# Kernel tuning notes

Measured on AMD Instinct MI355X. Metric: run time of the kernel, lower is better.

Reference implementation:

```python
import jax, jax.numpy as jnp
import numpy as np

MODES = 16
WIDTH = 64
SCHMIDT = 8
N_LAYERS = 4


def _spectral_conv(x, wr, wi, modes):
    """Quantum spectral conv: truncated 2D FFT -> complex Schmidt-rank einsum -> inverse FFT.
    x: (B,H,W,C) real. wr, wi: (modes,modes,C,C,S)."""
    b, H, W, C = x.shape
    S = wr.shape[-1]
    # quantum_fourier_modes: keep low (modes x modes) Fourier modes
    x_ft = jnp.fft.fftn(x, axes=(1, 2))[:, :modes, :modes, :]          # (B,m,n,C) complex
    w = wr + 1j * wi                                                     # (m,n,C,C,S)
    # tensor_product_einsum('b...nc,mncos->b...mos')
    out_ft = jnp.einsum('bxnc,mncos->bxmos', x_ft, w)                   # (B,m,m,C,S)
    # recombine Schmidt components (normalized sum over rank)
    out_ft = out_ft.sum(axis=-1) * (1.0 / float(np.sqrt(S)))            # (B,m,m,C)
    full = jnp.zeros((b, H, W, C), dtype=x_ft.dtype).at[:, :modes, :modes, :].set(out_ft)
    # inverse quantum_fourier_modes + .real
    return jnp.fft.ifftn(full, axes=(1, 2)).real


def setup_inputs() -> dict:
    key = jax.random.key(0)
    ks = jax.random.split(key, 12)
    B, H, W, Cin = 16, 128, 128, 3
    sc = 0.02
    inp = {
        'x': jax.random.normal(ks[0], (B, H, W, Cin), jnp.float32),
        'fc_in_w': jax.random.normal(ks[1], (Cin, WIDTH), jnp.float32) * sc,
        'fc_in_b': jnp.zeros((WIDTH,), jnp.float32),
        'wr': jax.random.normal(ks[2], (N_LAYERS, MODES, MODES, WIDTH, WIDTH, SCHMIDT), jnp.float32) * sc,
        'wi': jax.random.normal(ks[3], (N_LAYERS, MODES, MODES, WIDTH, WIDTH, SCHMIDT), jnp.float32) * sc,
        'ww': jax.random.normal(ks[4], (N_LAYERS, WIDTH, WIDTH), jnp.float32) * sc,
        'wb': jnp.zeros((N_LAYERS, WIDTH), jnp.float32),
        'fc1_w': jax.random.normal(ks[5], (WIDTH, 128), jnp.float32) * sc,
        'fc1_b': jnp.zeros((128,), jnp.float32),
        'fc2_w': jax.random.normal(ks[6], (128, 1), jnp.float32) * sc,
        'fc2_b': jnp.zeros((1,), jnp.float32),
    }
    return inp


def reference(x, fc_in_w, fc_in_b, wr, wi, ww, wb, fc1_w, fc1_b, fc2_w, fc2_b) -> jnp.ndarray:
    h = x @ fc_in_w + fc_in_b                                   # (B,H,W,width)
    for i in range(N_LAYERS):
        x1 = _spectral_conv(h, wr[i], wi[i], MODES)             # quantum spectral path
        x2 = h @ ww[i] + wb[i]                                  # pointwise Dense path
        h = jax.nn.gelu(x1 + x2)
    h = jax.nn.gelu(h @ fc1_w + fc1_b)
    return h @ fc2_w + fc2_b                                    # (B,H,W,1)
```

## Files before the change

### kernel.cpp

```cpp
#include <hip/hip_runtime.h>
#include <math.h>


#define TWO_PI_128 0.049087385212340517f
#define PI_4       0.78539816339744831f

__device__ __forceinline__ float gelu_f(float v) {
  float ex = 1.5957691216057308f * v * fmaf(0.044715f, v * v, 1.0f);
  float e = __expf(fminf(ex, 30.0f));
  float r = __builtin_amdgcn_rcpf(e + 1.0f);
  return fmaf(-v, r, v);
}

__global__ __launch_bounds__(256) void k_fc_in(const float* __restrict__ x,
    const float* __restrict__ w, const float* __restrict__ b,
    float* __restrict__ h) {
  int t = blockIdx.x * 256 + threadIdx.x;
  int pix = t >> 4, c4 = (t & 15) << 2;
  float x0 = x[pix * 3], x1 = x[pix * 3 + 1], x2 = x[pix * 3 + 2];
  float4 acc = *(const float4*)&b[c4];
  float4 w0 = *(const float4*)&w[c4];
  float4 w1 = *(const float4*)&w[64 + c4];
  float4 w2 = *(const float4*)&w[128 + c4];
  acc.x = fmaf(x2, w2.x, fmaf(x1, w1.x, fmaf(x0, w0.x, acc.x)));
  acc.y = fmaf(x2, w2.y, fmaf(x1, w1.y, fmaf(x0, w0.y, acc.y)));
  acc.z = fmaf(x2, w2.z, fmaf(x1, w1.z, fmaf(x0, w0.z, acc.z)));
  acc.w = fmaf(x2, w2.w, fmaf(x1, w1.w, fmaf(x0, w0.w, acc.w)));
  *(float4*)&h[(size_t)pix * 64 + c4] = acc;
}

__global__ __launch_bounds__(256) void k_prep(const float* __restrict__ wr,
    const float* __restrict__ wi, float* __restrict__ Br, float* __restrict__ Bi) {
  int t = blockIdx.x * 256 + threadIdx.x;
  int o = t & 63, c = (t >> 6) & 63, n = (t >> 12) & 15, m = t >> 16;
  const float4* pr = (const float4*)(wr) + (size_t)t * 2;
  float4 a = pr[0], d = pr[1];
  float sr = ((a.x + a.y) + (a.z + a.w)) + ((d.x + d.y) + (d.z + d.w));
  const float4* pi = (const float4*)(wi) + (size_t)t * 2;
  a = pi[0]; d = pi[1];
  float si = ((a.x + a.y) + (a.z + a.w)) + ((d.x + d.y) + (d.z + d.w));
  const float scale = 0.35355339059327373f / 16384.0f;
  int k = n * 64 + c, j = m * 64 + o;
  Br[k * 1024 + j] = sr * scale;
  Bi[k * 1024 + j] = si * scale;
}

__global__ __launch_bounds__(256) void k_dft_y(const float* __restrict__ h,
                                               float2* __restrict__ A1) {
  __shared__ float sh[128 * 64];
  int bx = blockIdx.x;
  const float* src = h + (size_t)bx * 8192;
  for (int i = threadIdx.x; i < 2048; i += 256)
    *(float4*)&sh[i * 4] = *(const float4*)&src[i * 4];
  __syncthreads();
  int c = threadIdx.x & 63, kg = threadIdx.x >> 6;
  float cs[4], sn[4], wr_[4], wi_[4], sr[4], si[4];
  #pragma unroll
  for (int q = 0; q < 4; ++q) {
    int ky = kg + 4 * q;
    __sincosf(-TWO_PI_128 * (float)ky, &sn[q], &cs[q]);
    wr_[q] = 1.f; wi_[q] = 0.f; sr[q] = 0.f; si[q] = 0.f;
  }
  for (int y = 0; y < 128; ++y) {
    float hv = sh[y * 64 + c];
    #pragma unroll
    for (int q = 0; q < 4; ++q) {
      sr[q] = fmaf(hv, wr_[q], sr[q]);
      si[q] = fmaf(hv, wi_[q], si[q]);
      float nw = wr_[q] * cs[q] - wi_[q] * sn[q];
      wi_[q] = fmaf(wi_[q], cs[q], wr_[q] * sn[q]);
      wr_[q] = nw;
    }
  }
  #pragma unroll
  for (int q = 0; q < 4; ++q) {
    int ky = kg + 4 * q;
    A1[((size_t)bx * 16 + ky) * 64 + c] = make_float2(sr[q], si[q]);
  }
}

__global__ __launch_bounds__(256) void k_dft_x(const float2* __restrict__ A1,
    float* __restrict__ Ar, float* __restrict__ Ai) {
  __shared__ float2 sh[128 * 32];
  int b = blockIdx.x, ky = blockIdx.y, ch = blockIdx.z;
  int c0 = ch * 32;
  for (int i = threadIdx.x; i < 2048; i += 256) {
    int xx = i >> 4, u = (i & 15) * 2;
    *(float4*)&sh[xx * 32 + u] =
        *(const float4*)&A1[(((size_t)b * 128 + xx) * 16 + ky) * 64 + c0 + u];
  }
  __syncthreads();
  int cl = threadIdx.x & 31, kxg = threadIdx.x >> 5;
  float cs[2], sn[2], wr_[2], wi_[2], sr[2], si[2];
  #pragma unroll
  for (int q = 0; q < 2; ++q) {
    int kx = kxg + 8 * q;
    __sincosf(-TWO_PI_128 * (float)kx, &sn[q], &cs[q]);
    wr_[q] = 1.f; wi_[q] = 0.f; sr[q] = 0.f; si[q] = 0.f;
  }
  for (int xx = 0; xx < 128; ++xx) {
    float2 v = sh[xx * 32 + cl];
    #pragma unroll
    for (int q = 0; q < 2; ++q) {
      sr[q] = fmaf(v.x, wr_[q], sr[q]); sr[q] = fmaf(-v.y, wi_[q], sr[q]);
      si[q] = fmaf(v.x, wi_[q], si[q]); si[q] = fmaf(v.y, wr_[q], si[q]);
      float nw = wr_[q] * cs[q] - wi_[q] * sn[q];
      wi_[q] = fmaf(wi_[q], cs[q], wr_[q] * sn[q]);
      wr_[q] = nw;
    }
  }
  #pragma unroll
  for (int q = 0; q < 2; ++q) {
    int kx = kxg + 8 * q;
    int row = b * 16 + kx, col = ky * 64 + c0 + cl;
    Ar[row * 1024 + col] = sr[q];
    Ai[row * 1024 + col] = si[q];
  }
}

__global__ __launch_bounds__(256) void k_gemm(const float* __restrict__ Ar,
    const float* __restrict__ Ai, const float* __restrict__ Br,
    const float* __restrict__ Bi, float2* __restrict__ Cp) {
  __shared__ float2 As[32][34];
  __shared__ float2 Bs[32][34];
  int tx = threadIdx.x & 15, ty = threadIdx.x >> 4;
  int row0 = blockIdx.y * 32, col0 = blockIdx.x * 32, kbase = blockIdx.z * 512;
  float cr00 = 0, cr01 = 0, cr10 = 0, cr11 = 0;
  float ci00 = 0, ci01 = 0, ci10 = 0, ci11 = 0;
  for (int kt = 0; kt < 512; kt += 32) {
    int k0 = kbase + kt;
    {
      int r = threadIdx.x >> 3, k4 = (threadIdx.x & 7) << 2;
      int gi = (row0 + r) * 1024 + k0 + k4;
      float4 ar = *(const float4*)&Ar[gi];
      float4 ai = *(const float4*)&Ai[gi];
      *(float4*)&As[r][k4]     = make_float4(ar.x, ai.x, ar.y, ai.y);
      *(float4*)&As[r][k4 + 2] = make_float4(ar.z, ai.z, ar.w, ai.w);
    }
    {
      int kk = threadIdx.x >> 3, j4 = (threadIdx.x & 7) << 2;
      int gi = (k0 + kk) * 1024 + col0 + j4;
      float4 br = *(const float4*)&Br[gi];
      float4 bi = *(const float4*)&Bi[gi];
      *(float4*)&Bs[kk][j4]     = make_float4(br.x, bi.x, br.y, bi.y);
      *(float4*)&Bs[kk][j4 + 2] = make_float4(br.z, bi.z, br.w, bi.w);
    }
    __syncthreads();
    #pragma unroll 8
    for (int kk = 0; kk < 32; ++kk) {
      float2 a0 = As[ty * 2][kk], a1 = As[ty * 2 + 1][kk];
      float2 b0 = Bs[kk][tx * 2], b1 = Bs[kk][tx * 2 + 1];
      cr00 = fmaf(a0.x, b0.x, cr00); cr00 = fmaf(-a0.y, b0.y, cr00);
      ci00 = fmaf(a0.x, b0.y, ci00); ci00 = fmaf(a0.y, b0.x, ci00);
      cr01 = fmaf(a0.x, b1.x, cr01); cr01 = fmaf(-a0.y, b1.y, cr01);
      ci01 = fmaf(a0.x, b1.y, ci01); ci01 = fmaf(a0.y, b1.x, ci01);
      cr10 = fmaf(a1.x, b0.x, cr10); cr10 = fmaf(-a1.y, b0.y, cr10);
      ci10 = fmaf(a1.x, b0.y, ci10); ci10 = fmaf(a1.y, b0.x, ci10);
      cr11 = fmaf(a1.x, b1.x, cr11); cr11 = fmaf(-a1.y, b1.y, cr11);
      ci11 = fmaf(a1.x, b1.y, ci11); ci11 = fmaf(a1.y, b1.x, ci11);
    }
    __syncthreads();
  }
  int r = row0 + ty * 2, jj = col0 + tx * 2;
  size_t base = ((size_t)blockIdx.z * 256 + r) * 1024 + jj;
  Cp[base]        = make_float2(cr00, ci00);
  Cp[base + 1]    = make_float2(cr01, ci01);
  Cp[base + 1024] = make_float2(cr10, ci10);
  Cp[base + 1025] = make_float2(cr11, ci11);
}

__global__ __launch_bounds__(256) void k_ifft_y(const float2* __restrict__ Cp,
                                                float2* __restrict__ T) {
  __shared__ float2 Cl[1024];
  int b = blockIdx.x >> 4, kx = blockIdx.x & 15;
  int row = b * 16 + kx;
  for (int i = threadIdx.x; i < 512; i += 256) {
    float4 u = *(const float4*)&Cp[(size_t)row * 1024 + i * 2];
    float4 v = *(const float4*)&Cp[(size_t)(256 + row) * 1024 + i * 2];
    *(float4*)&Cl[i * 2] = make_float4(u.x + v.x, u.y + v.y, u.z + v.z, u.w + v.w);
  }
  __syncthreads();
  int c = threadIdx.x & 63, yg = threadIdx.x >> 6;
  for (int y = yg; y < 128; y += 4) {
    float snv, csv;
    __sincosf(TWO_PI_128 * (float)y, &snv, &csv);
    float wr_ = 1.f, wi_ = 0.f, sr = 0.f, si = 0.f;
    #pragma unroll
    for (int ky = 0; ky < 16; ++ky) {
      float2 v = Cl[ky * 64 + c];
      sr = fmaf(v.x, wr_, sr); sr = fmaf(-v.y, wi_, sr);
      si = fmaf(v.x, wi_, si); si = fmaf(v.y, wr_, si);
      float nw = wr_ * csv - wi_ * snv;
      wi_ = fmaf(wi_, csv, wr_ * snv);
      wr_ = nw;
    }
    T[(((size_t)b * 128 + y) * 16 + kx) * 64 + c] = make_float2(sr, si);
  }
}

__global__ __launch_bounds__(256, 4) void k_layer_out(const float* hin,
    const float2* __restrict__ T, const float* __restrict__ ww,
    const float* __restrict__ wb, float* hout) {
  __shared__ alignas(16) float wwT[64 * 68];
  int b = blockIdx.x >> 7, y = blockIdx.x & 127;
  for (int i = threadIdx.x; i < 1024; i += 256) {
    int k = i >> 4, c4 = (i & 15) << 2;
    float4 v = *(const float4*)&ww[k * 64 + c4];
    wwT[(c4 + 0) * 68 + k] = v.x;
    wwT[(c4 + 1) * 68 + k] = v.y;
    wwT[(c4 + 2) * 68 + k] = v.z;
    wwT[(c4 + 3) * 68 + k] = v.w;
  }
  const float2* Tp = T + ((size_t)b * 128 + y) * 1024;
  __syncthreads();
  int ct = threadIdx.x & 15, xg = threadIdx.x >> 4;
  float acc[8][4];
  #pragma unroll
  for (int cc = 0; cc < 4; ++cc) {
    float bv = wb[ct + 16 * cc];
    #pragma unroll
    for (int j = 0; j < 8; ++j) acc[j][cc] = bv;
  }
  for (int kx = 0; kx < 16; ++kx) {
    float tr[4], ti[4];
    #pragma unroll
    for (int cc = 0; cc < 4; ++cc) {
      float2 v = Tp[kx * 64 + ct + 16 * cc];
      tr[cc] = v.x; ti[cc] = v.y;
    }
    float s0v, c0v, sst, cst;
    __sincosf(TWO_PI_128 * (float)(kx * xg), &s0v, &c0v);
    __sincosf(PI_4 * (float)kx, &sst, &cst);
    float wr_ = c0v, wi_ = s0v;
    #pragma unroll
    for (int j = 0; j < 8; ++j) {
      #pragma unroll
      for (int cc = 0; cc < 4; ++cc) {
        acc[j][cc] = fmaf(tr[cc], wr_, acc[j][cc]);
        acc[j][cc] = fmaf(-ti[cc], wi_, acc[j][cc]);
      }
      float nw = wr_ * cst - wi_ * sst;
      wi_ = fmaf(wi_, cst, wr_ * sst);
      wr_ = nw;
    }
  }
  const float* hrow = hin + (((size_t)b * 128 + xg) * 128 + y) * 64;
  #pragma unroll 1
  for (int kq = 0; kq < 64; kq += 4) {
    float4 wv[4];
    #pragma unroll
    for (int cc = 0; cc < 4; ++cc)
      wv[cc] = *(const float4*)&wwT[(ct + 16 * cc) * 68 + kq];
    #pragma unroll
    for (int j = 0; j < 8; ++j) {
      float4 hv = *(const float4*)&hrow[(size_t)j * 131072 + kq];
      #pragma unroll
      for (int cc = 0; cc < 4; ++cc) {
        acc[j][cc] = fmaf(hv.x, wv[cc].x, acc[j][cc]);
        acc[j][cc] = fmaf(hv.y, wv[cc].y, acc[j][cc]);
        acc[j][cc] = fmaf(hv.z, wv[cc].z, acc[j][cc]);
        acc[j][cc] = fmaf(hv.w, wv[cc].w, acc[j][cc]);
      }
    }
  }
  __syncthreads();
  #pragma unroll
  for (int j = 0; j < 8; ++j) {
    int xx = xg + 16 * j;
    size_t base = (((size_t)b * 128 + xx) * 128 + y) * 64 + ct;
    #pragma unroll
    for (int cc = 0; cc < 4; ++cc)
      hout[base + 16 * cc] = gelu_f(acc[j][cc]);
  }
}

__global__ __launch_bounds__(256, 3) void k_final(const float* __restrict__ h,
    const float* __restrict__ w1, const float* __restrict__ b1,
    const float* __restrict__ w2, const float* __restrict__ b2,
    float* __restrict__ out) {
  __shared__ alignas(16) float w1T[128 * 68];
  __shared__ float b1s[128];
  __shared__ float w2s[128];
  for (int i = threadIdx.x; i < 2048; i += 256) {
    int k = i >> 5, j4 = (i & 31) << 2;
    float4 v = *(const float4*)&w1[k * 128 + j4];
    w1T[(j4 + 0) * 68 + k] = v.x;
    w1T[(j4 + 1) * 68 + k] = v.y;
    w1T[(j4 + 2) * 68 + k] = v.z;
    w1T[(j4 + 3) * 68 + k] = v.w;
  }
  if (threadIdx.x < 128) {
    b1s[threadIdx.x] = b1[threadIdx.x];
    w2s[threadIdx.x] = w2[threadIdx.x];
  }
  __syncthreads();
  int jt = threadIdx.x & 15, rg = threadIdx.x >> 4;
  int r0 = blockIdx.x * 128;
  const float* hb = h + (size_t)(r0 + rg) * 64;
  float acc[8][8];
  #pragma unroll
  for (int cc = 0; cc < 8; ++cc) {
    float bv = b1s[jt + 16 * cc];
    #pragma unroll
    for (int ii = 0; ii < 8; ++ii) acc[ii][cc] = bv;
  }
  float4 hv[8], hn[8];
  #pragma unroll
  for (int ii = 0; ii < 8; ++ii) hv[ii] = *(const float4*)&hb[ii * 1024];

  auto fmab = [&](const float4* H, int kq) {
    #pragma unroll
    for (int cc = 0; cc < 8; ++cc) {
      float4 wv = *(const float4*)&w1T[(jt + 16 * cc) * 68 + kq];
      #pragma unroll
      for (int ii = 0; ii < 8; ++ii) {
        acc[ii][cc] = fmaf(H[ii].x, wv.x, acc[ii][cc]);
        acc[ii][cc] = fmaf(H[ii].y, wv.y, acc[ii][cc]);
        acc[ii][cc] = fmaf(H[ii].z, wv.z, acc[ii][cc]);
        acc[ii][cc] = fmaf(H[ii].w, wv.w, acc[ii][cc]);
      }
    }
  };
  #pragma unroll 1
  for (int kq = 0; kq < 64; kq += 8) {
    #pragma unroll
    for (int ii = 0; ii < 8; ++ii)
      hn[ii] = *(const float4*)&hb[ii * 1024 + kq + 4];
    fmab(hv, kq);
    #pragma unroll
    for (int ii = 0; ii < 8; ++ii)
      hv[ii] = *(const float4*)&hb[ii * 1024 + kq + 8];
    fmab(hn, kq + 4);
  }
  float b2v = b2[0];
  #pragma unroll
  for (int ii = 0; ii < 8; ++ii) {
    float part = 0.f;
    #pragma unroll
    for (int cc = 0; cc < 8; ++cc)
      part = fmaf(gelu_f(acc[ii][cc]), w2s[jt + 16 * cc], part);
    part += __shfl_xor(part, 1, 64);
    part += __shfl_xor(part, 2, 64);
    part += __shfl_xor(part, 4, 64);
    part += __shfl_xor(part, 8, 64);
    if (jt == 0) out[r0 + rg + 16 * ii] = part + b2v;
  }
}

extern "C" void kernel_launch(void* const* d_in, const int* in_sizes, int n_in,
                              void* d_out, int out_size, void* d_ws, size_t ws_size,
                              hipStream_t stream) {
  (void)in_sizes; (void)n_in; (void)out_size; (void)ws_size;
  const float* x      = (const float*)d_in[0];
  const float* fcin_w = (const float*)d_in[1];
  const float* fcin_b = (const float*)d_in[2];
  const float* wr     = (const float*)d_in[3];
  const float* wi     = (const float*)d_in[4];
  const float* ww     = (const float*)d_in[5];
  const float* wb     = (const float*)d_in[6];
  const float* fc1_w  = (const float*)d_in[7];
  const float* fc1_b  = (const float*)d_in[8];
  const float* fc2_w  = (const float*)d_in[9];
  const float* fc2_b  = (const float*)d_in[10];
  float* out = (float*)d_out;

  float*  hA = (float*)d_ws;
  float2* A1 = (float2*)(hA + 16777216);
  float*  Ar = (float*)(A1 + 2097152);
  float*  Ai = Ar + 262144;
  float*  Br = Ai + 262144;
  float*  Bi = Br + 1048576;
  float2* Cp = (float2*)(Bi + 1048576);

  k_fc_in<<<16384, 256, 0, stream>>>(x, fcin_w, fcin_b, hA);
  for (int l = 0; l < 4; ++l) {
    k_prep<<<4096, 256, 0, stream>>>(wr + (size_t)l * 8388608,
                                     wi + (size_t)l * 8388608, Br, Bi);
    k_dft_y<<<2048, 256, 0, stream>>>(hA, A1);
    k_dft_x<<<dim3(16, 16, 2), 256, 0, stream>>>(A1, Ar, Ai);
    k_gemm<<<dim3(32, 8, 2), 256, 0, stream>>>(Ar, Ai, Br, Bi, Cp);
    k_ifft_y<<<256, 256, 0, stream>>>(Cp, A1);
    k_layer_out<<<2048, 256, 0, stream>>>(hA, A1, ww + (size_t)l * 4096,
                                          wb + (size_t)l * 64, hA);
  }
  k_final<<<2048, 256, 0, stream>>>(hA, fc1_w, fc1_b, fc2_w, fc2_b, out);
}
```

Before: 1.115 ms.

## Radix-4 split y-DFT, double-buffer complex GEMM tiles, stage h in LDS for final MLP

The y-direction DFT kernel now splits the 128-point sum into four interleaved 32-point partial sums that share one twiddle recurrence, then combines them with a small radix-4 twiddle step. This cuts the per-sample twiddle rotation work by about four times at the cost of more live registers. The complex GEMM gains a double-buffered LDS tile with register prefetch of the next K slice, so global loads overlap the FMA loop. The final MLP kernel stages its 128-row h tile into padded LDS with coalesced loads instead of strided per-thread register prefetch, and drops the occupancy hint from its launch bounds.

```diff
diff --git a/kernel.cpp b/kernel.cpp
--- a/kernel.cpp
+++ b/kernel.cpp
@@ -54,28 +54,48 @@
     *(float4*)&sh[i * 4] = *(const float4*)&src[i * 4];
   __syncthreads();
   int c = threadIdx.x & 63, kg = threadIdx.x >> 6;
-  float cs[4], sn[4], wr_[4], wi_[4], sr[4], si[4];
+  float s4r[4][4], s4i[4][4];
+  float w4r[4], w4i[4], c4t[4], s4t[4];
   #pragma unroll
   for (int q = 0; q < 4; ++q) {
     int ky = kg + 4 * q;
-    __sincosf(-TWO_PI_128 * (float)ky, &sn[q], &cs[q]);
-    wr_[q] = 1.f; wi_[q] = 0.f; sr[q] = 0.f; si[q] = 0.f;
-  }
-  for (int y = 0; y < 128; ++y) {
-    float hv = sh[y * 64 + c];
+    __sincosf(-TWO_PI_128 * 4.0f * (float)ky, &s4t[q], &c4t[q]);
+    w4r[q] = 1.f; w4i[q] = 0.f;
+    #pragma unroll
+    for (int p = 0; p < 4; ++p) { s4r[q][p] = 0.f; s4i[q][p] = 0.f; }
+  }
+  for (int m = 0; m < 32; ++m) {
+    float hv[4];
+    #pragma unroll
+    for (int p = 0; p < 4; ++p) hv[p] = sh[(4 * m + p) * 64 + c];
     #pragma unroll
     for (int q = 0; q < 4; ++q) {
-      sr[q] = fmaf(hv, wr_[q], sr[q]);
-      si[q] = fmaf(hv, wi_[q], si[q]);
-      float nw = wr_[q] * cs[q] - wi_[q] * sn[q];
-      wi_[q] = fmaf(wi_[q], cs[q], wr_[q] * sn[q]);
-      wr_[q] = nw;
+      #pragma unroll
+      for (int p = 0; p < 4; ++p) {
+        s4r[q][p] = fmaf(hv[p], w4r[q], s4r[q][p]);
+        s4i[q][p] = fmaf(hv[p], w4i[q], s4i[q][p]);
+      }
+      float nw = w4r[q] * c4t[q] - w4i[q] * s4t[q];
+      w4i[q] = fmaf(w4i[q], c4t[q], w4r[q] * s4t[q]);
+      w4r[q] = nw;
     }
   }
   #pragma unroll
   for (int q = 0; q < 4; ++q) {
     int ky = kg + 4 * q;
-    A1[((size_t)bx * 16 + ky) * 64 + c] = make_float2(sr[q], si[q]);
+    float s1, c1;
+    __sincosf(-TWO_PI_128 * (float)ky, &s1, &c1);
+    float sr = s4r[q][0], si = s4i[q][0];
+    float wr_ = c1, wi_ = s1;
+    #pragma unroll
+    for (int p = 1; p < 4; ++p) {
+      sr = fmaf(s4r[q][p], wr_, sr); sr = fmaf(-s4i[q][p], wi_, sr);
+      si = fmaf(s4r[q][p], wi_, si); si = fmaf(s4i[q][p], wr_, si);
+      float nw = wr_ * c1 - wi_ * s1;
+      wi_ = fmaf(wi_, c1, wr_ * s1);
+      wr_ = nw;
+    }
+    A1[((size_t)bx * 16 + ky) * 64 + c] = make_float2(sr, si);
   }
 }
 
@@ -121,35 +141,42 @@
 __global__ __launch_bounds__(256) void k_gemm(const float* __restrict__ Ar,
     const float* __restrict__ Ai, const float* __restrict__ Br,
     const float* __restrict__ Bi, float2* __restrict__ Cp) {
-  __shared__ float2 As[32][34];
-  __shared__ float2 Bs[32][34];
+  __shared__ float2 As[2][32][34];
+  __shared__ float2 Bs[2][32][34];
   int tx = threadIdx.x & 15, ty = threadIdx.x >> 4;
   int row0 = blockIdx.y * 32, col0 = blockIdx.x * 32, kbase = blockIdx.z * 512;
+  int ra = threadIdx.x >> 3, k4 = (threadIdx.x & 7) << 2;
+  float4 arv, aiv, brv, biv;
   float cr00 = 0, cr01 = 0, cr10 = 0, cr11 = 0;
   float ci00 = 0, ci01 = 0, ci10 = 0, ci11 = 0;
-  for (int kt = 0; kt < 512; kt += 32) {
-    int k0 = kbase + kt;
-    {
-      int r = threadIdx.x >> 3, k4 = (threadIdx.x & 7) << 2;
-      int gi = (row0 + r) * 1024 + k0 + k4;
-      float4 ar = *(const float4*)&Ar[gi];
-      float4 ai = *(const float4*)&Ai[gi];
-      *(float4*)&As[r][k4]     = make_float4(ar.x, ai.x, ar.y, ai.y);
-      *(float4*)&As[r][k4 + 2] = make_float4(ar.z, ai.z, ar.w, ai.w);
-    }
-    {
-      int kk = threadIdx.x >> 3, j4 = (threadIdx.x & 7) << 2;
-      int gi = (k0 + kk) * 1024 + col0 + j4;
-      float4 br = *(const float4*)&Br[gi];
-      float4 bi = *(const float4*)&Bi[gi];
-      *(float4*)&Bs[kk][j4]     = make_float4(br.x, bi.x, br.y, bi.y);
-      *(float4*)&Bs[kk][j4 + 2] = make_float4(br.z, bi.z, br.w, bi.w);
-    }
-    __syncthreads();
+  {
+    int gia = (row0 + ra) * 1024 + kbase + k4;
+    arv = *(const float4*)&Ar[gia];
+    aiv = *(const float4*)&Ai[gia];
+    int gib = (kbase + ra) * 1024 + col0 + k4;
+    brv = *(const float4*)&Br[gib];
+    biv = *(const float4*)&Bi[gib];
+    *(float4*)&As[0][ra][k4]     = make_float4(arv.x, aiv.x, arv.y, aiv.y);
+    *(float4*)&As[0][ra][k4 + 2] = make_float4(arv.z, aiv.z, arv.w, aiv.w);
+    *(float4*)&Bs[0][ra][k4]     = make_float4(brv.x, biv.x, brv.y, biv.y);
+    *(float4*)&Bs[0][ra][k4 + 2] = make_float4(brv.z, biv.z, brv.w, biv.w);
+  }
+  __syncthreads();
+  for (int kt = 0; kt < 16; ++kt) {
+    if (kt < 15) {
+      int k0 = kbase + (kt + 1) * 32;
+      int gia = (row0 + ra) * 1024 + k0 + k4;
+      arv = *(const float4*)&Ar[gia];
+      aiv = *(const float4*)&Ai[gia];
+      int gib = (k0 + ra) * 1024 + col0 + k4;
+      brv = *(const float4*)&Br[gib];
+      biv = *(const float4*)&Bi[gib];
+    }
+    int cur = kt & 1;
     #pragma unroll 8
     for (int kk = 0; kk < 32; ++kk) {
-      float2 a0 = As[ty * 2][kk], a1 = As[ty * 2 + 1][kk];
-      float2 b0 = Bs[kk][tx * 2], b1 = Bs[kk][tx * 2 + 1];
+      float2 a0 = As[cur][ty * 2][kk], a1 = As[cur][ty * 2 + 1][kk];
+      float2 b0 = Bs[cur][kk][tx * 2], b1 = Bs[cur][kk][tx * 2 + 1];
       cr00 = fmaf(a0.x, b0.x, cr00); cr00 = fmaf(-a0.y, b0.y, cr00);
       ci00 = fmaf(a0.x, b0.y, ci00); ci00 = fmaf(a0.y, b0.x, ci00);
       cr01 = fmaf(a0.x, b1.x, cr01); cr01 = fmaf(-a0.y, b1.y, cr01);
@@ -158,6 +185,14 @@
       ci10 = fmaf(a1.x, b0.y, ci10); ci10 = fmaf(a1.y, b0.x, ci10);
       cr11 = fmaf(a1.x, b1.x, cr11); cr11 = fmaf(-a1.y, b1.y, cr11);
       ci11 = fmaf(a1.x, b1.y, ci11); ci11 = fmaf(a1.y, b1.x, ci11);
+    }
+    __syncthreads();
+    if (kt < 15) {
+      int nxt = cur ^ 1;
+      *(float4*)&As[nxt][ra][k4]     = make_float4(arv.x, aiv.x, arv.y, aiv.y);
+      *(float4*)&As[nxt][ra][k4 + 2] = make_float4(arv.z, aiv.z, arv.w, aiv.w);
+      *(float4*)&Bs[nxt][ra][k4]     = make_float4(brv.x, biv.x, brv.y, biv.y);
+      *(float4*)&Bs[nxt][ra][k4 + 2] = make_float4(brv.z, biv.z, brv.w, biv.w);
     }
     __syncthreads();
   }
@@ -274,29 +309,30 @@
   }
 }
 
-__global__ __launch_bounds__(256, 3) void k_final(const float* __restrict__ h,
+__global__ __launch_bounds__(256) void k_final(const float* __restrict__ h,
     const float* __restrict__ w1, const float* __restrict__ b1,
     const float* __restrict__ w2, const float* __restrict__ b2,
     float* __restrict__ out) {
   __shared__ alignas(16) float w1T[128 * 68];
+  __shared__ alignas(16) float hl[128 * 68];
   __shared__ float b1s[128];
   __shared__ float w2s[128];
-  for (int i = threadIdx.x; i < 2048; i += 256) {
-    int k = i >> 5, j4 = (i & 31) << 2;
-    float4 v = *(const float4*)&w1[k * 128 + j4];
-    w1T[(j4 + 0) * 68 + k] = v.x;
-    w1T[(j4 + 1) * 68 + k] = v.y;
-    w1T[(j4 + 2) * 68 + k] = v.z;
-    w1T[(j4 + 3) * 68 + k] = v.w;
+  for (int i = threadIdx.x; i < 8192; i += 256) {
+    int k = i >> 7, j = i & 127;
+    w1T[j * 68 + k] = w1[i];
   }
   if (threadIdx.x < 128) {
     b1s[threadIdx.x] = b1[threadIdx.x];
     w2s[threadIdx.x] = w2[threadIdx.x];
   }
+  int r0 = blockIdx.x * 128;
+  for (int i = threadIdx.x; i < 2048; i += 256) {
+    int r = i >> 4, kq = (i & 15) * 4;
+    float4 v = *(const float4*)&h[(size_t)(r0 + r) * 64 + kq];
+    *(float4*)&hl[r * 68 + kq] = v;
+  }
   __syncthreads();
   int jt = threadIdx.x & 15, rg = threadIdx.x >> 4;
-  int r0 = blockIdx.x * 128;
-  const float* hb = h + (size_t)(r0 + rg) * 64;
   float acc[8][8];
   #pragma unroll
   for (int cc = 0; cc < 8; ++cc) {
@@ -304,33 +340,23 @@
     #pragma unroll
     for (int ii = 0; ii < 8; ++ii) acc[ii][cc] = bv;
   }
-  float4 hv[8], hn[8];
-  #pragma unroll
-  for (int ii = 0; ii < 8; ++ii) hv[ii] = *(const float4*)&hb[ii * 1024];
-
-  auto fmab = [&](const float4* H, int kq) {
+  #pragma unroll 1
+  for (int kq = 0; kq < 64; kq += 4) {
+    float4 hv[8];
+    #pragma unroll
+    for (int ii = 0; ii < 8; ++ii)
+      hv[ii] = *(const float4*)&hl[(rg + 16 * ii) * 68 + kq];
     #pragma unroll
     for (int cc = 0; cc < 8; ++cc) {
       float4 wv = *(const float4*)&w1T[(jt + 16 * cc) * 68 + kq];
       #pragma unroll
       for (int ii = 0; ii < 8; ++ii) {
-        acc[ii][cc] = fmaf(H[ii].x, wv.x, acc[ii][cc]);
-        acc[ii][cc] = fmaf(H[ii].y, wv.y, acc[ii][cc]);
-        acc[ii][cc] = fmaf(H[ii].z, wv.z, acc[ii][cc]);
-        acc[ii][cc] = fmaf(H[ii].w, wv.w, acc[ii][cc]);
+        acc[ii][cc] = fmaf(hv[ii].x, wv.x, acc[ii][cc]);
+        acc[ii][cc] = fmaf(hv[ii].y, wv.y, acc[ii][cc]);
+        acc[ii][cc] = fmaf(hv[ii].z, wv.z, acc[ii][cc]);
+        acc[ii][cc] = fmaf(hv[ii].w, wv.w, acc[ii][cc]);
       }
     }
-  };
-  #pragma unroll 1
-  for (int kq = 0; kq < 64; kq += 8) {
-    #pragma unroll
-    for (int ii = 0; ii < 8; ++ii)
-      hn[ii] = *(const float4*)&hb[ii * 1024 + kq + 4];
-    fmab(hv, kq);
-    #pragma unroll
-    for (int ii = 0; ii < 8; ++ii)
-      hv[ii] = *(const float4*)&hb[ii * 1024 + kq + 8];
-    fmab(hn, kq + 4);
   }
   float b2v = b2[0];
   #pragma unroll
```

Result: faster. 1.015 ms (-8.9%).
